# Kernel tuning notes

Measured on AMD Instinct MI355X. Metric: run time of the kernel, lower is better.

Reference implementation:

```python
import jax, jax.numpy as jnp
import numpy as np
from jax import lax

B, C, H, W = 8, 64, 112, 112
MID = 256
K = 5
DIL = 2
PAD = 4


def setup_inputs() -> dict:
    key = jax.random.key(0)
    k1, k2, k3, k4, k5 = jax.random.split(key, 5)
    x = jax.random.normal(k1, (B, C, H, W), dtype=jnp.float32)
    # conv1: in_channel -> 256, k=5, dilation=2, pad=4
    w1 = jax.random.normal(k2, (MID, C, K, K), dtype=jnp.float32) * (1.0 / np.sqrt(C * K * K))
    b1 = jax.random.normal(k3, (MID,), dtype=jnp.float32) * 0.01
    # conv2: 256 -> 25, 1x1
    w2 = jax.random.normal(k4, (K * K, MID, 1, 1), dtype=jnp.float32) * (1.0 / np.sqrt(MID))
    b2 = jax.random.normal(k5, (K * K,), dtype=jnp.float32) * 0.01
    return {"x": x, "w1": w1, "b1": b1, "w2": w2, "b2": b2}


def reference(x, w1, b1, w2, b2):
    # attention-weight branch
    k = lax.conv_general_dilated(
        x, w1, window_strides=(1, 1), padding=[(PAD, PAD), (PAD, PAD)],
        rhs_dilation=(DIL, DIL), dimension_numbers=("NCHW", "OIHW", "NCHW"))
    k = k + b1[None, :, None, None]                       # [B, 256, H, W]
    k = jnp.einsum("oi,bihw->bohw", w2[:, :, 0, 0], k) + b2[None, :, None, None]
    k = jax.nn.softmax(k, axis=1)                          # [B, 25, H, W]

    # fused local attention: weighted sum over the 5x5 dilated neighborhood.
    # Equivalent to unfold(x, k=5, dilation=2, pad=4) * k summed over the 25 taps,
    # but never materializes the [B, C, 25, H, W] unfolded tensor.
    xp = jnp.pad(x, ((0, 0), (0, 0), (PAD, PAD), (PAD, PAD)))
    out = jnp.zeros_like(x)
    for idx in range(K * K):
        i, j = divmod(idx, K)
        patch = lax.dynamic_slice(xp, (0, 0, DIL * i, DIL * j), (B, C, H, W))
        out = out + patch * k[:, idx:idx + 1]              # broadcast over C
    return out
```

## Files before the change

### kernel.cpp

```cpp
#include <hip/hip_runtime.h>

#define BATCH 8
#define CH    64
#define HH    112
#define WW    112
#define HW    (HH * WW)
#define NP    (BATCH * HW)
#define TAPS  25
#define MIDC  256
#define PIX   64
#define CPW   16
#define NBLK  (NP / PIX)
#define NXCD  8
#define CPX   (NBLK / NXCD)

#define WEFF_N (CH * TAPS * TAPS)
__global__ __launch_bounds__(256) void weff_kernel(
    const float* __restrict__ w1, const float* __restrict__ b1,
    const float* __restrict__ w2, const float* __restrict__ b2,
    float* __restrict__ weff, float* __restrict__ beff) {
  const int id = blockIdx.x * 256 + threadIdx.x;
  if (id < WEFF_N) {
    const int tap = id % TAPS;
    const int t2  = id / TAPS;
    const int o   = t2 % TAPS;
    const int c   = t2 / TAPS;
    const float* w2o = w2 + o * MIDC;
    float a0 = 0.f, a1 = 0.f;
    #pragma unroll 4
    for (int mid = 0; mid < MIDC; mid += 2) {
      a0 = fmaf(w1[(mid * CH + c) * TAPS + tap],       w2o[mid],     a0);
      a1 = fmaf(w1[((mid + 1) * CH + c) * TAPS + tap], w2o[mid + 1], a1);
    }
    weff[(c * TAPS + tap) * TAPS + o] = a0 + a1;
  } else if (id < WEFF_N + TAPS) {
    const int o = id - WEFF_N;
    const float* w2o = w2 + o * MIDC;
    float b = b2[o];
    for (int mid = 0; mid < MIDC; ++mid) b = fmaf(w2o[mid], b1[mid], b);
    beff[o] = b;
  }
}

__global__ __launch_bounds__(256, 6) void picanet_main(
    const float* __restrict__ x, const float* __restrict__ weff,
    const float* __restrict__ beff, float* __restrict__ out) {
  __shared__ float red[2 * PIX * TAPS];

  const int lane = threadIdx.x & 63;
  const int wave = threadIdx.x >> 6;
  const int c0 = __builtin_amdgcn_readfirstlane(wave * CPW);

  const int lb = (blockIdx.x & (NXCD - 1)) * CPX + (blockIdx.x >> 3);
  const int p  = lb * PIX + lane;
  const int b  = p / HW;
  const int hw = p % HW;
  const int h  = hw / WW;
  const int w  = hw % WW;

  const float* xb = x + (size_t)b * CH * HW + (size_t)c0 * HW;
  const float* wc = weff + (size_t)c0 * TAPS * TAPS;

  float s[TAPS];
  #pragma unroll
  for (int o = 0; o < TAPS; ++o) s[o] = 0.f;

  #pragma unroll 1
  for (int tap = 0; tap < TAPS; ++tap) {
    int i = tap / 5, j = tap % 5;
    int yy = h + 2 * i - 4;
    int xx = w + 2 * j - 4;
    if (yy >= 0 && yy < HH && xx >= 0 && xx < WW) {
      const float* xp = xb + yy * WW + xx;
      float xv[CPW];
      #pragma unroll
      for (int c = 0; c < CPW; ++c) xv[c] = xp[(size_t)c * HW];
      const float* wt = wc + tap * TAPS;
      #pragma unroll
      for (int c = 0; c < CPW; ++c) {
        const float* wp = wt + c * (TAPS * TAPS);
        #pragma unroll
        for (int o = 0; o < TAPS; ++o) s[o] = fmaf(xv[c], wp[o], s[o]);
      }
    }
  }

  if (wave >= 2) {
    float* dst = red + (wave - 2) * (PIX * TAPS);
    #pragma unroll
    for (int o = 0; o < TAPS; ++o) dst[lane * TAPS + o] = s[o];
  }
  __syncthreads();
  if (wave < 2) {
    const float* srcp = red + wave * (PIX * TAPS);
    #pragma unroll
    for (int o = 0; o < TAPS; ++o) s[o] += srcp[lane * TAPS + o];
  }
  if (wave == 1) {
    float* dst = red + (PIX * TAPS);
    #pragma unroll
    for (int o = 0; o < TAPS; ++o) dst[lane * TAPS + o] = s[o];
  }
  __syncthreads();

  if (wave == 0) {
    const float* srcp = red + (PIX * TAPS);
    float t[TAPS];
    #pragma unroll
    for (int o = 0; o < TAPS; ++o)
      t[o] = s[o] + srcp[lane * TAPS + o] + beff[o];
    float m = t[0];
    #pragma unroll
    for (int o = 1; o < TAPS; ++o) m = fmaxf(m, t[o]);
    float sum = 0.f;
    #pragma unroll
    for (int o = 0; o < TAPS; ++o) { t[o] = __expf(t[o] - m); sum += t[o]; }
    float inv = 1.f / sum;
    #pragma unroll
    for (int o = 0; o < TAPS; ++o) red[lane * TAPS + o] = t[o] * inv;
  }
  __syncthreads();

  float acc[CPW];
  #pragma unroll
  for (int c = 0; c < CPW; ++c) acc[c] = 0.f;

  #pragma unroll 1
  for (int tap = 0; tap < TAPS; ++tap) {
    int i = tap / 5, j = tap % 5;
    int yy = h + 2 * i - 4;
    int xx = w + 2 * j - 4;
    float sv = red[lane * TAPS + tap];
    if (yy >= 0 && yy < HH && xx >= 0 && xx < WW) {
      const float* xp = xb + yy * WW + xx;
      #pragma unroll
      for (int c = 0; c < CPW; ++c)
        acc[c] = fmaf(sv, xp[(size_t)c * HW], acc[c]);
    }
  }

  float* ob = out + (size_t)b * CH * HW + (size_t)c0 * HW + hw;
  #pragma unroll
  for (int c = 0; c < CPW; ++c) ob[c * HW] = acc[c];
}

extern "C" void kernel_launch(void* const* d_in, const int* in_sizes, int n_in,
                              void* d_out, int out_size, void* d_ws, size_t ws_size,
                              hipStream_t stream) {
  const float* x  = (const float*)d_in[0];
  const float* w1 = (const float*)d_in[1];
  const float* b1 = (const float*)d_in[2];
  const float* w2 = (const float*)d_in[3];
  const float* b2 = (const float*)d_in[4];
  float* out  = (float*)d_out;
  float* weff = (float*)d_ws;
  float* beff = weff + CH * TAPS * TAPS;

  weff_kernel<<<(WEFF_N + TAPS + 255) / 256, 256, 0, stream>>>(w1, b1, w2, b2, weff, beff);
  picanet_main<<<NBLK, 256, 0, stream>>>(x, weff, beff, out);
}
```

Baseline: 220.2 us.

## Transpose input to NHWC and use float4 channel loads in main kernel

Adds a transpose kernel that writes x into an NHWC workspace buffer. The main kernel then reads each wave's 16 channels per tap with four float4 loads instead of 16 strided scalar loads. The change targets poorly coalesced gathers across channel planes. In exchange it adds an extra kernel launch and a full read and write of x, about 25 MB. It falls back to the old NCHW path when the workspace is too small.

```diff
diff --git a/kernel.cpp b/kernel.cpp
--- a/kernel.cpp
+++ b/kernel.cpp
@@ -13,6 +13,7 @@
 #define NBLK  (NP / PIX)
 #define NXCD  8
 #define CPX   (NBLK / NXCD)
+#define TILES_PER_IMG (HW / PIX)
 
 #define WEFF_N (CH * TAPS * TAPS)
 __global__ __launch_bounds__(256) void weff_kernel(
@@ -42,8 +43,29 @@
   }
 }
 
-__global__ __launch_bounds__(256, 6) void picanet_main(
-    const float* __restrict__ x, const float* __restrict__ weff,
+__global__ __launch_bounds__(256) void xpose_kernel(
+    const float* __restrict__ x, float* __restrict__ xt) {
+  __shared__ float tile[CH][PIX + 1];
+  const int b  = blockIdx.x / TILES_PER_IMG;
+  const int p0 = (blockIdx.x % TILES_PER_IMG) * PIX;
+  const int tid = threadIdx.x;
+  const int lo = tid & 63;
+  const int g  = tid >> 6;
+  #pragma unroll
+  for (int k = 0; k < 16; ++k) {
+    int c = (g << 4) + k;
+    tile[c][lo] = x[((size_t)b * CH + c) * HW + p0 + lo];
+  }
+  __syncthreads();
+  #pragma unroll
+  for (int k = 0; k < 16; ++k) {
+    int px = (g << 4) + k;
+    xt[((size_t)(b * HW + p0 + px)) * CH + lo] = tile[lo][px];
+  }
+}
+
+__global__ __launch_bounds__(256, 6) void picanet_nhwc(
+    const float* __restrict__ xt, const float* __restrict__ weff,
     const float* __restrict__ beff, float* __restrict__ out) {
   __shared__ float red[2 * PIX * TAPS];
 
@@ -58,8 +80,125 @@
   const int h  = hw / WW;
   const int w  = hw % WW;
 
+  const float* xb = xt + ((size_t)b * HW) * CH + c0;
+  const float* wc = weff + (size_t)c0 * (TAPS * TAPS);
+
+  float s[TAPS];
+  #pragma unroll
+  for (int o = 0; o < TAPS; ++o) s[o] = 0.f;
+
+  #pragma unroll 1
+  for (int tap = 0; tap < TAPS; ++tap) {
+    int i = tap / 5, j = tap % 5;
+    int yy = h + 2 * i - 4;
+    int xx = w + 2 * j - 4;
+    if (yy >= 0 && yy < HH && xx >= 0 && xx < WW) {
+      const float* xp = xb + (size_t)(yy * WW + xx) * CH;
+      float4 q0 = *(const float4*)(xp);
+      float4 q1 = *(const float4*)(xp + 4);
+      float4 q2 = *(const float4*)(xp + 8);
+      float4 q3 = *(const float4*)(xp + 12);
+      float xv[CPW];
+      xv[0]=q0.x;  xv[1]=q0.y;  xv[2]=q0.z;  xv[3]=q0.w;
+      xv[4]=q1.x;  xv[5]=q1.y;  xv[6]=q1.z;  xv[7]=q1.w;
+      xv[8]=q2.x;  xv[9]=q2.y;  xv[10]=q2.z; xv[11]=q2.w;
+      xv[12]=q3.x; xv[13]=q3.y; xv[14]=q3.z; xv[15]=q3.w;
+      const float* wt = wc + tap * TAPS;
+      #pragma unroll
+      for (int c = 0; c < CPW; ++c) {
+        const float* wp = wt + c * (TAPS * TAPS);
+        #pragma unroll
+        for (int o = 0; o < TAPS; ++o) s[o] = fmaf(xv[c], wp[o], s[o]);
+      }
+    }
+  }
+
+  if (wave >= 2) {
+    float* dst = red + (wave - 2) * (PIX * TAPS);
+    #pragma unroll
+    for (int o = 0; o < TAPS; ++o) dst[lane * TAPS + o] = s[o];
+  }
+  __syncthreads();
+  if (wave < 2) {
+    const float* srcp = red + wave * (PIX * TAPS);
+    #pragma unroll
+    for (int o = 0; o < TAPS; ++o) s[o] += srcp[lane * TAPS + o];
+  }
+  if (wave == 1) {
+    float* dst = red + (PIX * TAPS);
+    #pragma unroll
+    for (int o = 0; o < TAPS; ++o) dst[lane * TAPS + o] = s[o];
+  }
+  __syncthreads();
+
+  if (wave == 0) {
+    const float* srcp = red + (PIX * TAPS);
+    float t[TAPS];
+    #pragma unroll
+    for (int o = 0; o < TAPS; ++o)
+      t[o] = s[o] + srcp[lane * TAPS + o] + beff[o];
+    float m = t[0];
+    #pragma unroll
+    for (int o = 1; o < TAPS; ++o) m = fmaxf(m, t[o]);
+    float sum = 0.f;
+    #pragma unroll
+    for (int o = 0; o < TAPS; ++o) { t[o] = __expf(t[o] - m); sum += t[o]; }
+    float inv = 1.f / sum;
+    #pragma unroll
+    for (int o = 0; o < TAPS; ++o) red[lane * TAPS + o] = t[o] * inv;
+  }
+  __syncthreads();
+
+  float acc[CPW];
+  #pragma unroll
+  for (int c = 0; c < CPW; ++c) acc[c] = 0.f;
+
+  #pragma unroll 1
+  for (int tap = 0; tap < TAPS; ++tap) {
+    int i = tap / 5, j = tap % 5;
+    int yy = h + 2 * i - 4;
+    int xx = w + 2 * j - 4;
+    float sv = red[lane * TAPS + tap];
+    if (yy >= 0 && yy < HH && xx >= 0 && xx < WW) {
+      const float* xp = xb + (size_t)(yy * WW + xx) * CH;
+      float4 q0 = *(const float4*)(xp);
+      float4 q1 = *(const float4*)(xp + 4);
+      float4 q2 = *(const float4*)(xp + 8);
+      float4 q3 = *(const float4*)(xp + 12);
+      float xv[CPW];
+      xv[0]=q0.x;  xv[1]=q0.y;  xv[2]=q0.z;  xv[3]=q0.w;
+      xv[4]=q1.x;  xv[5]=q1.y;  xv[6]=q1.z;  xv[7]=q1.w;
+      xv[8]=q2.x;  xv[9]=q2.y;  xv[10]=q2.z; xv[11]=q2.w;
+      xv[12]=q3.x; xv[13]=q3.y; xv[14]=q3.z; xv[15]=q3.w;
+      #pragma unroll
+      for (int c = 0; c < CPW; ++c)
+        acc[c] = fmaf(sv, xv[c], acc[c]);
+    }
+  }
+
+  float* ob = out + (size_t)b * CH * HW + (size_t)c0 * HW + hw;
+  #pragma unroll
+  for (int c = 0; c < CPW; ++c) ob[c * HW] = acc[c];
+}
+
+__global__ __launch_bounds__(256, 6) void picanet_nchw(
+    const float* __restrict__ x, const float* __restrict__ weff,
+    const float* __restrict__ beff, float* __restrict__ out) {
+  __shared__ float red[2 * PIX * TAPS];
+
+  const int lane = threadIdx.x & 63;
+  const int wave = threadIdx.x >> 6;
+  const int c0 = __builtin_amdgcn_readfirstlane(wave * CPW);
+
+  const int lb = (blockIdx.x & (NXCD - 1)) * CPX + (blockIdx.x >> 3);
+  const int p  = lb * PIX + lane;
+  const int b  = p / HW;
+  const int hw = p % HW;
+  const int h  = hw / WW;
+  const int w  = hw % WW;
+
   const float* xb = x + (size_t)b * CH * HW + (size_t)c0 * HW;
-  const float* wc = weff + (size_t)c0 * TAPS * TAPS;
+  const float* wc = weff + (size_t)c0 * (TAPS * TAPS);
 
   float s[TAPS];
   #pragma unroll
@@ -152,10 +291,22 @@
   const float* b1 = (const float*)d_in[2];
   const float* w2 = (const float*)d_in[3];
   const float* b2 = (const float*)d_in[4];
-  float* out  = (float*)d_out;
-  float* weff = (float*)d_ws;
-  float* beff = weff + CH * TAPS * TAPS;
-
-  weff_kernel<<<(WEFF_N + TAPS + 255) / 256, 256, 0, stream>>>(w1, b1, w2, b2, weff, beff);
-  picanet_main<<<NBLK, 256, 0, stream>>>(x, weff, beff, out);
-}
+  float* out = (float*)d_out;
+
+  const size_t xt_floats = (size_t)NP * CH;
+  const size_t need = (xt_floats + WEFF_N + TAPS) * sizeof(float);
+  const bool nhwc = (ws_size >= need);
+
+  float* xt   = (float*)d_ws;
+  float* weff = nhwc ? (xt + xt_floats) : (float*)d_ws;
+  float* beff = weff + WEFF_N;
+
+  weff_kernel<<<(WEFF_N + TAPS + 255) / 256, 256, 0, stream>>>(
+      w1, b1, w2, b2, weff, beff);
+  if (nhwc) {
+    xpose_kernel<<<NBLK, 256, 0, stream>>>(x, xt);
+    picanet_nhwc<<<NBLK, 256, 0, stream>>>(xt, weff, beff, out);
+  } else {
+    picanet_nchw<<<NBLK, 256, 0, stream>>>(x, weff, beff, out);
+  }
+}
```

After: 274.4 us. +24.6%, slower.
